# Performance work log

Hardware: AMD Instinct MI355X
Metric: run time of the kernel (lower is better)

Reference implementation:

```python
import jax, jax.numpy as jnp
import numpy as np

# ---- config (matches init_kwargs) ----
DIM = 2048
N_HEADS = 16
Q_LORA = 1536
KV_LORA = 512
QK_NOPE = 128
QK_ROPE = 64
V_HEAD = 128
QK_HEAD = QK_NOPE + QK_ROPE  # 192
B, S = 2, 2048
EPS = 1e-6


def rmsnorm(x, w):
    return x * jax.lax.rsqrt(jnp.mean(x * x, axis=-1, keepdims=True) + EPS) * w


def apply_rotary_emb(x, freqs_cis):
    # x: (B, S, H, R) interleaved pairs; freqs_cis: (S, R//2, 2) = (cos, sin)
    xr = x.astype(jnp.float32).reshape(x.shape[:-1] + (-1, 2))
    cos = freqs_cis[None, :, None, :, 0]
    sin = freqs_cis[None, :, None, :, 1]
    out = jnp.stack(
        [xr[..., 0] * cos - xr[..., 1] * sin,
         xr[..., 1] * cos + xr[..., 0] * sin], axis=-1)
    return out.reshape(x.shape).astype(x.dtype)


def setup_inputs() -> dict:
    key = jax.random.key(0)
    ks = jax.random.split(key, 12)
    sc = lambda fan_in: 1.0 / np.sqrt(fan_in)

    x = jax.random.normal(ks[0], (B, S, DIM), jnp.float32)

    # RoPE table: (S, QK_ROPE//2, 2)
    inv_freq = 1.0 / (10000.0 ** (jnp.arange(0, QK_ROPE, 2, dtype=jnp.float32) / QK_ROPE))
    t = jnp.arange(S, dtype=jnp.float32)
    ang = jnp.einsum('s,r->sr', t, inv_freq)
    freqs_cis = jnp.stack([jnp.cos(ang), jnp.sin(ang)], axis=-1)

    # causal mask (S, T)
    mask = jnp.triu(jnp.full((S, S), -jnp.inf, dtype=jnp.float32), 1)

    params = {
        'wq_a_w': jax.random.normal(ks[1], (Q_LORA, DIM), jnp.float32) * sc(DIM),
        'wq_a_b': jnp.zeros((Q_LORA,), jnp.float32),
        'q_norm_w': jnp.ones((Q_LORA,), jnp.float32),
        'wq_b_w': jax.random.normal(ks[2], (N_HEADS * QK_HEAD, Q_LORA), jnp.float32) * sc(Q_LORA),
        'wq_b_b': jnp.zeros((N_HEADS * QK_HEAD,), jnp.float32),
        'wkv_a_w': jax.random.normal(ks[3], (KV_LORA + QK_ROPE, DIM), jnp.float32) * sc(DIM),
        'wkv_a_b': jnp.zeros((KV_LORA + QK_ROPE,), jnp.float32),
        'kv_norm_w': jnp.ones((KV_LORA,), jnp.float32),
        'wkv_b_w': jax.random.normal(ks[4], (N_HEADS * (QK_NOPE + V_HEAD), KV_LORA), jnp.float32) * sc(KV_LORA),
        'wo_w': jax.random.normal(ks[5], (DIM, N_HEADS * V_HEAD), jnp.float32) * sc(N_HEADS * V_HEAD),
        'wo_b': jnp.zeros((DIM,), jnp.float32),
    }
    return {'x': x, 'freqs_cis': freqs_cis, 'mask': mask, 'start_pos': 0, **params}


def reference(x, freqs_cis, mask, wq_a_w, wq_a_b, q_norm_w, wq_b_w, wq_b_b,
              wkv_a_w, wkv_a_b, kv_norm_w, wkv_b_w, wo_w, wo_b, start_pos):
    bsz, seqlen, _ = x.shape
    scale = QK_HEAD ** (-0.5)

    # q path (low-rank)
    q = rmsnorm(x @ wq_a_w.T + wq_a_b, q_norm_w) @ wq_b_w.T + wq_b_b
    q = q.reshape(bsz, seqlen, N_HEADS, QK_HEAD)
    q_nope, q_pe = q[..., :QK_NOPE], q[..., QK_NOPE:]
    q_pe = apply_rotary_emb(q_pe, freqs_cis)

    # kv path
    kv = x @ wkv_a_w.T + wkv_a_b
    kv, k_pe = kv[..., :KV_LORA], kv[..., KV_LORA:]
    k_pe = apply_rotary_emb(k_pe[:, :, None, :], freqs_cis)[:, :, 0, :]  # (B,T,R)

    # absorption: fold W_UK into q_nope
    wkv_b = wkv_b_w.reshape(N_HEADS, QK_NOPE + V_HEAD, KV_LORA)
    q_nope = jnp.einsum('bshd,hdc->bshc', q_nope, wkv_b[:, :QK_NOPE])
    kv_cache = rmsnorm(kv, kv_norm_w)  # (B,T,C)

    scores = (jnp.einsum('bshc,btc->bsht', q_nope, kv_cache)
              + jnp.einsum('bshr,btr->bsht', q_pe, k_pe)) * scale
    scores = scores + mask[:, None, :]
    attn = jax.nn.softmax(scores.astype(jnp.float32), axis=-1).astype(x.dtype)

    out = jnp.einsum('bsht,btc->bshc', attn, kv_cache)
    out = jnp.einsum('bshc,hdc->bshd', out, wkv_b[:, -V_HEAD:])
    out = out.reshape(bsz, seqlen, N_HEADS * V_HEAD) @ wo_w.T + wo_b
    return out
```

## Files before the change

### kernel.cpp

```cpp
#include <hip/hip_runtime.h>
#include <math.h>

#define B_    2
#define S_    2048
#define M_TOT 4096
#define DIM_  2048
#define NH_   16
#define QL_   1536
#define KVL_  512
#define QKN_  128
#define QKR_  64
#define VH_   128
#define QKH_  192
#define QSTR  3072
#define QP_STR 584

typedef short s16x8 __attribute__((ext_vector_type(8)));
typedef float f32x4 __attribute__((ext_vector_type(4)));
typedef unsigned short u16;
#define AS1 __attribute__((address_space(1)))
#define AS3 __attribute__((address_space(3)))

__device__ inline u16 f2bf(float f) {
    unsigned u = __float_as_uint(f);
    unsigned r = u + 0x7FFFu + ((u >> 16) & 1u);
    return (u16)(r >> 16);
}
__device__ inline float bf2f(u16 h) { return __uint_as_float(((unsigned)h) << 16); }

__device__ __forceinline__ void ld_lds16(const u16* g, u16* l) {
    __builtin_amdgcn_global_load_lds((const AS1 unsigned*)g, (AS3 unsigned*)l, 16, 0, 0);
}
__device__ __forceinline__ void bar_vm() {
    asm volatile("s_waitcnt vmcnt(0)" ::: "memory");
    __builtin_amdgcn_s_barrier();
}
__device__ __forceinline__ void bar_lgkm() {
    asm volatile("s_waitcnt lgkmcnt(0)" ::: "memory");
    __builtin_amdgcn_s_barrier();
}
__device__ __forceinline__ void bar_all() {
    asm volatile("s_waitcnt vmcnt(0) lgkmcnt(0)" ::: "memory");
    __builtin_amdgcn_s_barrier();
}

__global__ __launch_bounds__(256)
void gemm_bf16(const u16* __restrict__ A, const u16* __restrict__ Bm,
               const float* __restrict__ bias, void* __restrict__ Cv,
               int M, int N, int K, int ldA, int ldB, int ldC,
               long long sAz, long long sBz, long long sCz,
               float alpha, int outF32)
{
    __shared__ u16 As[128 * 32];
    __shared__ u16 Bs[128 * 32];
    const int tid = threadIdx.x;
    const int w = tid >> 6, l = tid & 63;
    const int m0 = blockIdx.y * 128, n0 = blockIdx.x * 128;
    const int z = blockIdx.z;
    const u16* Az = A + (size_t)z * sAz;
    const u16* Bz = Bm + (size_t)z * sBz;

    const int rin = l >> 2;
    const int cel = (l & 3) * 8;
    const int lane15 = l & 15, quad = l >> 4;
    const int wm = w & 1, wn = w >> 1;

    f32x4 acc[4][4] = {};

    for (int k0 = 0; k0 < K; k0 += 32) {
        __syncthreads();
        #pragma unroll
        for (int c = 0; c < 2; ++c) {
            const int chunk = w * 2 + c;
            const int rowA = m0 + chunk * 16 + rin;
            const u16* ga = Az + (size_t)rowA * ldA + k0 + cel;
            u16* la = &As[chunk * 512 + rin * 32 + cel];
            __builtin_amdgcn_global_load_lds((const AS1 unsigned*)ga, (AS3 unsigned*)la, 16, 0, 0);
            int rowB = n0 + chunk * 16 + rin;
            if (rowB > N - 1) rowB = N - 1;
            const u16* gb = Bz + (size_t)rowB * ldB + k0 + cel;
            u16* lb = &Bs[chunk * 512 + rin * 32 + cel];
            __builtin_amdgcn_global_load_lds((const AS1 unsigned*)gb, (AS3 unsigned*)lb, 16, 0, 0);
        }
        __syncthreads();
        s16x8 af[4], bf[4];
        #pragma unroll
        for (int i = 0; i < 4; ++i)
            af[i] = *(const s16x8*)&As[(wm * 64 + i * 16 + lane15) * 32 + quad * 8];
        #pragma unroll
        for (int i = 0; i < 4; ++i)
            bf[i] = *(const s16x8*)&Bs[(wn * 64 + i * 16 + lane15) * 32 + quad * 8];
        #pragma unroll
        for (int mi = 0; mi < 4; ++mi)
            #pragma unroll
            for (int ni = 0; ni < 4; ++ni)
                acc[mi][ni] = __builtin_amdgcn_mfma_f32_16x16x32_bf16(af[mi], bf[ni], acc[mi][ni], 0, 0, 0);
    }

    const int cmb = m0 + wm * 64, cnb = n0 + wn * 64;
    if (outF32) {
        float* C = (float*)Cv + (size_t)z * sCz;
        #pragma unroll
        for (int mi = 0; mi < 4; ++mi)
            #pragma unroll
            for (int ni = 0; ni < 4; ++ni) {
                const int nn = cnb + ni * 16 + lane15;
                if (nn < N) {
                    const float bv = bias ? bias[nn] : 0.f;
                    #pragma unroll
                    for (int r = 0; r < 4; ++r) {
                        const int mm = cmb + mi * 16 + quad * 4 + r;
                        C[(size_t)mm * ldC + nn] = acc[mi][ni][r] * alpha + bv;
                    }
                }
            }
    } else {
        u16* C = (u16*)Cv + (size_t)z * sCz;
        #pragma unroll
        for (int mi = 0; mi < 4; ++mi)
            #pragma unroll
            for (int ni = 0; ni < 4; ++ni) {
                const int nn = cnb + ni * 16 + lane15;
                if (nn < N) {
                    const float bv = bias ? bias[nn] : 0.f;
                    #pragma unroll
                    for (int r = 0; r < 4; ++r) {
                        const int mm = cmb + mi * 16 + quad * 4 + r;
                        C[(size_t)mm * ldC + nn] = f2bf(acc[mi][ni][r] * alpha + bv);
                    }
                }
            }
    }
}

__global__ __launch_bounds__(512)
void mla_flash(u16* __restrict__ Qp, const u16* __restrict__ Kcat,
               const u16* __restrict__ KVT)
{
    __shared__ u16 sQ[64 * QP_STR];
    __shared__ u16 sKV[2][16384];
    __shared__ u16 sP[64 * 136];
    __shared__ float sRm[64 * 4];
    __shared__ float sRs[64 * 4];
    __shared__ float sM[64], sL[64];

    const int tid = threadIdx.x;
    const int w = tid >> 6, l = tid & 63;
    const int lane15 = l & 15, quad = l >> 4;
    const int wq = w & 1;
    const int wk = w >> 1;

    const int flat = blockIdx.x;
    const int xcd  = flat & 7;
    const int slot = flat >> 3;
    const int b    = xcd >> 2;
    const int h    = (xcd & 3) * 4 + (slot & 3);
    const int qt   = 31 - (slot >> 2);

    const int qs = qt * 64;
    u16* Qrow = Qp + ((size_t)h * M_TOT + b * S_ + qs) * 576;
    const float scale = 0.07216878364870323f;
    const u16* Kb = Kcat + (size_t)b * S_ * 576;
    const u16* Vb = KVT + (size_t)b * 512 * S_;

    const int key = tid >> 2;
    const int seg8 = (tid & 3) * 8;
    const int sx8  = (((tid & 3) ^ ((tid >> 3) & 3)) * 8);
    const int qx8  = ((quad ^ ((lane15 >> 1) & 3)) * 8);
    const int ktiles = (qs + 191) >> 7;

    auto stageK = [&](int kt, int j, int buf) {
        #pragma unroll
        for (int kk = 0; kk < 3; ++kk) {
            const u16* g = Kb + (size_t)(kt + key) * 576 + j * 96 + kk * 32 + sx8;
            ld_lds16(g, &sKV[buf][kk * 4096 + key * 32 + seg8]);
        }
    };
    auto stageV = [&](int kt, int tc, int buf) {
        #pragma unroll
        for (int jj = 0; jj < 4; ++jj) {
            const int c = jj * 128 + key;
            const u16* g = Vb + (size_t)c * S_ + kt + tc * 32 + sx8;
            ld_lds16(g, &sKV[buf][jj * 4096 + key * 32 + seg8]);
        }
    };

    stageK(0, 0, 0);
    {
        const int r = tid >> 3, c0 = (tid & 7) * 8;
        #pragma unroll
        for (int jj = 0; jj < 9; ++jj) {
            const int c = c0 + jj * 64;
            *(s16x8*)&sQ[r * QP_STR + c] = *(const s16x8*)&Qrow[(size_t)r * 576 + c];
        }
    }
    if (tid < 64) { sM[tid] = -1e30f; sL[tid] = 0.f; }
    bar_all();

    f32x4 Oacc[2][8] = {};
    float mn_[2][4], al_[2][4];

    for (int kt0 = 0; kt0 < ktiles; ++kt0) {
        const int kt = kt0 << 7;
        f32x4 Sacc[2][2] = {};

        #pragma unroll
        for (int j = 0; j < 6; ++j) {
            const int cur = j & 1;
            if (j < 5) stageK(kt, j + 1, cur ^ 1);
            else       stageV(kt, 0, 0);
            __builtin_amdgcn_s_setprio(1);
            #pragma unroll
            for (int kk = 0; kk < 3; ++kk) {
                s16x8 af[2], bf[2];
                #pragma unroll
                for (int mi = 0; mi < 2; ++mi)
                    af[mi] = *(const s16x8*)&sQ[(wq * 32 + mi * 16 + lane15) * QP_STR + j * 96 + kk * 32 + quad * 8];
                #pragma unroll
                for (int ni = 0; ni < 2; ++ni)
                    bf[ni] = *(const s16x8*)&sKV[cur][kk * 4096 + (wk * 32 + ni * 16 + lane15) * 32 + qx8];
                #pragma unroll
                for (int mi = 0; mi < 2; ++mi)
                    #pragma unroll
                    for (int ni = 0; ni < 2; ++ni)
                        Sacc[mi][ni] = __builtin_amdgcn_mfma_f32_16x16x32_bf16(af[mi], bf[ni], Sacc[mi][ni], 0, 0, 0);
            }
            __builtin_amdgcn_s_setprio(0);
            if (j < 5) bar_vm();
        }

        #pragma unroll
        for (int mi = 0; mi < 2; ++mi)
            #pragma unroll
            for (int r = 0; r < 4; ++r) {
                const int rowl = wq * 32 + mi * 16 + quad * 4 + r;
                const int rowg = qs + rowl;
                float mx = -1e30f;
                #pragma unroll
                for (int ni = 0; ni < 2; ++ni) {
                    const int colg = kt + wk * 32 + ni * 16 + lane15;
                    float v = Sacc[mi][ni][r] * scale;
                    v = (colg <= rowg) ? v : -1e30f;
                    Sacc[mi][ni][r] = v;
                    mx = fmaxf(mx, v);
                }
                #pragma unroll
                for (int sh = 1; sh < 16; sh <<= 1) mx = fmaxf(mx, __shfl_xor(mx, sh));
                if (lane15 == 0) sRm[rowl * 4 + wk] = mx;
            }
        bar_lgkm();

        #pragma unroll
        for (int mi = 0; mi < 2; ++mi)
            #pragma unroll
            for (int r = 0; r < 4; ++r) {
                const int rowl = wq * 32 + mi * 16 + quad * 4 + r;
                const f32x4 pm = *(const f32x4*)&sRm[rowl * 4];
                const float m_old = sM[rowl];
                const float mn = fmaxf(fmaxf(fmaxf(pm[0], pm[1]), fmaxf(pm[2], pm[3])), m_old);
                const float al = __expf(m_old - mn);
                mn_[mi][r] = mn; al_[mi][r] = al;
                float sum = 0.f;
                #pragma unroll
                for (int ni = 0; ni < 2; ++ni) {
                    const float p = __expf(Sacc[mi][ni][r] - mn);
                    sP[rowl * 136 + wk * 32 + ni * 16 + lane15] = f2bf(p);
                    sum += p;
                }
                #pragma unroll
                for (int ci = 0; ci < 8; ++ci) Oacc[mi][ci][r] *= al;
                #pragma unroll
                for (int sh = 1; sh < 16; sh <<= 1) sum += __shfl_xor(sum, sh);
                if (lane15 == 0) sRs[rowl * 4 + wk] = sum;
            }
        bar_all();

        if (wk == 0 && lane15 == 0) {
            #pragma unroll
            for (int mi = 0; mi < 2; ++mi)
                #pragma unroll
                for (int r = 0; r < 4; ++r) {
                    const int rowl = wq * 32 + mi * 16 + quad * 4 + r;
                    const f32x4 ps = *(const f32x4*)&sRs[rowl * 4];
                    sL[rowl] = sL[rowl] * al_[mi][r] + (ps[0] + ps[1] + ps[2] + ps[3]);
                    sM[rowl] = mn_[mi][r];
                }
        }

        #pragma unroll
        for (int tc = 0; tc < 4; ++tc) {
            const int cur = tc & 1;
            if (tc < 3)                 stageV(kt, tc + 1, cur ^ 1);
            else if (kt0 + 1 < ktiles)  stageK(kt + 128, 0, 0);
            s16x8 pf[2], vf[8];
            #pragma unroll
            for (int mi = 0; mi < 2; ++mi)
                pf[mi] = *(const s16x8*)&sP[(wq * 32 + mi * 16 + lane15) * 136 + tc * 32 + quad * 8];
            #pragma unroll
            for (int ci = 0; ci < 8; ++ci)
                vf[ci] = *(const s16x8*)&sKV[cur][(wk * 128 + ci * 16 + lane15) * 32 + qx8];
            __builtin_amdgcn_s_setprio(1);
            #pragma unroll
            for (int mi = 0; mi < 2; ++mi)
                #pragma unroll
                for (int ci = 0; ci < 8; ++ci)
                    Oacc[mi][ci] = __builtin_amdgcn_mfma_f32_16x16x32_bf16(pf[mi], vf[ci], Oacc[mi][ci], 0, 0, 0);
            __builtin_amdgcn_s_setprio(0);
            bar_vm();
        }
    }

    bar_lgkm();
    #pragma unroll
    for (int mi = 0; mi < 2; ++mi)
        #pragma unroll
        for (int r = 0; r < 4; ++r) {
            const int rowl = wq * 32 + mi * 16 + quad * 4 + r;
            const float inv = 1.f / sL[rowl];
            #pragma unroll
            for (int ci = 0; ci < 8; ++ci)
                Qrow[(size_t)rowl * 576 + wk * 128 + ci * 16 + lane15] =
                    f2bf(Oacc[mi][ci][r] * inv);
        }
}

__global__ __launch_bounds__(256)
void cast_f32_bf16(const float* __restrict__ src, u16* __restrict__ dst, int n)
{
    for (int i = blockIdx.x * 256 + threadIdx.x; i < n; i += gridDim.x * 256)
        dst[i] = f2bf(src[i]);
}

__global__ __launch_bounds__(256)
void prep_wbnT(const float* __restrict__ wkvb, u16* __restrict__ dst)
{
    int i = blockIdx.x * 256 + threadIdx.x;
    int h = i >> 16, rem = i & 65535, c = rem >> 7, d = rem & 127;
    dst[i] = f2bf(wkvb[(size_t)(h * 256 + d) * 512 + c]);
}

__global__ __launch_bounds__(256)
void prep_wbv(const float* __restrict__ wkvb, u16* __restrict__ dst)
{
    int i = blockIdx.x * 256 + threadIdx.x;
    int h = i >> 16, rem = i & 65535;
    dst[i] = f2bf(wkvb[(size_t)h * 131072 + 65536 + rem]);
}

__global__ __launch_bounds__(256)
void rmsnorm_bf16(u16* __restrict__ X, const float* __restrict__ w, int D)
{
    const int m = blockIdx.x;
    u16* x = X + (size_t)m * D;
    float ss = 0.f;
    for (int k = threadIdx.x; k < D; k += 256) { float v = bf2f(x[k]); ss += v * v; }
    __shared__ float red[256];
    red[threadIdx.x] = ss; __syncthreads();
    for (int s = 128; s > 0; s >>= 1) {
        if (threadIdx.x < s) red[threadIdx.x] += red[threadIdx.x + s];
        __syncthreads();
    }
    const float sc = rsqrtf(red[0] / (float)D + 1e-6f);
    for (int k = threadIdx.x; k < D; k += 256) x[k] = f2bf(bf2f(x[k]) * sc * w[k]);
}

__global__ __launch_bounds__(256)
void rope_q(const u16* __restrict__ q, const float* __restrict__ freqs, u16* __restrict__ Qp)
{
    const int idx = blockIdx.x * 256 + threadIdx.x;
    const int i = idx & 31, h = (idx >> 5) & 15, m = idx >> 9;
    const int s = m & (S_ - 1);
    const float c = freqs[(s * 32 + i) * 2], sn = freqs[(s * 32 + i) * 2 + 1];
    const u16* src = q + (size_t)m * QSTR + h * QKH_ + QKN_ + 2 * i;
    const float x0 = bf2f(src[0]), x1 = bf2f(src[1]);
    u16* dst = Qp + ((size_t)h * M_TOT + m) * 576 + 512 + 2 * i;
    dst[0] = f2bf(x0 * c - x1 * sn);
    dst[1] = f2bf(x1 * c + x0 * sn);
}

__global__ __launch_bounds__(256)
void kv_norm_rope(const u16* __restrict__ kva, const float* __restrict__ w,
                  const float* __restrict__ freqs, u16* __restrict__ Kcat)
{
    const int m = blockIdx.x, s = m & (S_ - 1);
    const u16* x = kva + (size_t)m * 576;
    float ss = 0.f;
    for (int k = threadIdx.x; k < 512; k += 256) { float v = bf2f(x[k]); ss += v * v; }
    __shared__ float red[256];
    red[threadIdx.x] = ss; __syncthreads();
    for (int st = 128; st > 0; st >>= 1) {
        if (threadIdx.x < st) red[threadIdx.x] += red[threadIdx.x + st];
        __syncthreads();
    }
    const float sc = rsqrtf(red[0] / 512.f + 1e-6f);
    for (int k = threadIdx.x; k < 512; k += 256)
        Kcat[(size_t)m * 576 + k] = f2bf(bf2f(x[k]) * sc * w[k]);
    if (threadIdx.x < 32) {
        const int i = threadIdx.x;
        const float c = freqs[(s * 32 + i) * 2], sn = freqs[(s * 32 + i) * 2 + 1];
        const float x0 = bf2f(x[512 + 2 * i]), x1 = bf2f(x[512 + 2 * i + 1]);
        Kcat[(size_t)m * 576 + 512 + 2 * i]     = f2bf(x0 * c - x1 * sn);
        Kcat[(size_t)m * 576 + 512 + 2 * i + 1] = f2bf(x1 * c + x0 * sn);
    }
}

__global__ __launch_bounds__(256)
void transpose_kv(const u16* __restrict__ Kcat, u16* __restrict__ KVT)
{
    __shared__ u16 t[64][65];
    const int s0 = blockIdx.x * 64, c0 = blockIdx.y * 64, b = blockIdx.z;
    #pragma unroll
    for (int i = 0; i < 16; ++i) {
        int id = i * 256 + threadIdx.x, r = id >> 6, c = id & 63;
        t[r][c] = Kcat[(size_t)(b * S_ + s0 + r) * 576 + c0 + c];
    }
    __syncthreads();
    #pragma unroll
    for (int i = 0; i < 16; ++i) {
        int id = i * 256 + threadIdx.x, r = id >> 6, c = id & 63;
        KVT[(size_t)(b * 512 + c0 + r) * S_ + s0 + c] = t[c][r];
    }
}

extern "C" void kernel_launch(void* const* d_in, const int* in_sizes, int n_in,
                              void* d_out, int out_size, void* d_ws, size_t ws_size,
                              hipStream_t stream)
{
    (void)in_sizes; (void)n_in; (void)out_size; (void)ws_size;
    const float* x         = (const float*)d_in[0];
    const float* freqs     = (const float*)d_in[1];
    const float* wq_a_w    = (const float*)d_in[4];
    const float* wq_a_b    = (const float*)d_in[5];
    const float* q_norm_w  = (const float*)d_in[6];
    const float* wq_b_w    = (const float*)d_in[7];
    const float* wq_b_b    = (const float*)d_in[8];
    const float* wkv_a_w   = (const float*)d_in[9];
    const float* wkv_a_b   = (const float*)d_in[10];
    const float* kv_norm_w = (const float*)d_in[11];
    const float* wkv_b_w   = (const float*)d_in[12];
    const float* wo_w      = (const float*)d_in[13];
    const float* wo_b      = (const float*)d_in[14];
    float* out = (float*)d_out;

    char* W = (char*)d_ws;
    u16* x_bf  = (u16*)(W + 0);
    u16* wqa   = (u16*)(W + 16777216);
    u16* wqb   = (u16*)(W + 23068672);
    u16* wkva  = (u16*)(W + 32505856);
    u16* wobf  = (u16*)(W + 34865152);
    u16* wbnT  = (u16*)(W + 43253760);
    u16* wbv   = (u16*)(W + 45350912);
    u16* q_a   = (u16*)(W + 47448064);
    u16* q     = (u16*)(W + 60030976);
    u16* kv_a  = (u16*)(W + 85196800);
    u16* Kcat  = (u16*)(W + 89915392);
    u16* KVT   = (u16*)(W + 94633984);
    u16* Qp    = (u16*)(W + 98828288);
    u16* outh  = (u16*)(W + 174325760);

    const dim3 blk(256);

    cast_f32_bf16<<<2048, blk, 0, stream>>>(x, x_bf, M_TOT * DIM_);
    cast_f32_bf16<<<2048, blk, 0, stream>>>(wq_a_w, wqa, QL_ * DIM_);
    cast_f32_bf16<<<2048, blk, 0, stream>>>(wq_b_w, wqb, QSTR * QL_);
    cast_f32_bf16<<<2048, blk, 0, stream>>>(wkv_a_w, wkva, 576 * DIM_);
    cast_f32_bf16<<<2048, blk, 0, stream>>>(wo_w, wobf, DIM_ * DIM_);
    prep_wbnT<<<4096, blk, 0, stream>>>(wkv_b_w, wbnT);
    prep_wbv<<<4096, blk, 0, stream>>>(wkv_b_w, wbv);

    gemm_bf16<<<dim3(12, 32, 1), blk, 0, stream>>>(x_bf, wqa, wq_a_b, q_a,
        M_TOT, QL_, DIM_, DIM_, DIM_, QL_, 0, 0, 0, 1.f, 0);
    rmsnorm_bf16<<<M_TOT, blk, 0, stream>>>(q_a, q_norm_w, QL_);
    gemm_bf16<<<dim3(24, 32, 1), blk, 0, stream>>>(q_a, wqb, wq_b_b, q,
        M_TOT, QSTR, QL_, QL_, QL_, QSTR, 0, 0, 0, 1.f, 0);
    rope_q<<<(M_TOT * NH_ * 32) / 256, blk, 0, stream>>>(q, freqs, Qp);

    gemm_bf16<<<dim3(5, 32, 1), blk, 0, stream>>>(x_bf, wkva, wkv_a_b, kv_a,
        M_TOT, 576, DIM_, DIM_, DIM_, 576, 0, 0, 0, 1.f, 0);
    kv_norm_rope<<<M_TOT, blk, 0, stream>>>(kv_a, kv_norm_w, freqs, Kcat);
    transpose_kv<<<dim3(32, 8, 2), blk, 0, stream>>>(Kcat, KVT);

    gemm_bf16<<<dim3(4, 32, 16), blk, 0, stream>>>(q, wbnT, nullptr, Qp,
        M_TOT, 512, 128, QSTR, 128, 576, QKH_, 65536, (long long)M_TOT * 576, 1.f, 0);

    mla_flash<<<dim3(1024, 1, 1), dim3(512), 0, stream>>>(Qp, Kcat, KVT);

    gemm_bf16<<<dim3(1, 32, 16), blk, 0, stream>>>(Qp, wbv, nullptr, outh,
        M_TOT, VH_, 512, 576, 512, DIM_, (long long)M_TOT * 576, 65536, VH_, 1.f, 0);

    gemm_bf16<<<dim3(16, 32, 1), blk, 0, stream>>>(outh, wobf, wo_b, out,
        M_TOT, DIM_, DIM_, DIM_, DIM_, DIM_, 0, 0, 0, 1.f, 1);
}
```

Before: 851.1 us.

## Shrink MLA flash tile to 32 query rows and skip masked key sub-tiles

The flash attention kernel now uses 32-row query tiles with 256 threads and launches twice as many blocks. Each of the four waves owns a 32-key slice for QK and a 64-column slice of V. Key and V sub-tiles that lie fully beyond the causal diagonal are no longer staged or multiplied, and the K/V double buffer carries parity across tiles. The softmax switches to exp2 with a log2e-folded scale and skips rescaling the output accumulator when the running max has not grown past a threshold. The aim is finer causal work skipping, better load balance and less rescale work, at the cost of less Q reuse per K/V load and more blocks and barriers.

```diff
diff --git a/kernel.cpp b/kernel.cpp
--- a/kernel.cpp
+++ b/kernel.cpp
@@ -133,56 +133,59 @@
     }
 }
 
-__global__ __launch_bounds__(512)
+__global__ __launch_bounds__(256)
 void mla_flash(u16* __restrict__ Qp, const u16* __restrict__ Kcat,
                const u16* __restrict__ KVT)
 {
-    __shared__ u16 sQ[64 * QP_STR];
-    __shared__ u16 sKV[2][16384];
-    __shared__ u16 sP[64 * 136];
-    __shared__ float sRm[64 * 4];
-    __shared__ float sRs[64 * 4];
-    __shared__ float sM[64], sL[64];
+    __shared__ u16 sQ[32 * QP_STR];
+    __shared__ u16 sKV[2][8192];
+    __shared__ u16 sP[32 * 136];
+    __shared__ float sRm[32 * 4];
+    __shared__ float sRs[32 * 4];
+    __shared__ float sM[32], sL[32];
 
     const int tid = threadIdx.x;
     const int w = tid >> 6, l = tid & 63;
     const int lane15 = l & 15, quad = l >> 4;
-    const int wq = w & 1;
-    const int wk = w >> 1;
 
     const int flat = blockIdx.x;
     const int xcd  = flat & 7;
     const int slot = flat >> 3;
     const int b    = xcd >> 2;
     const int h    = (xcd & 3) * 4 + (slot & 3);
-    const int qt   = 31 - (slot >> 2);
-
-    const int qs = qt * 64;
+    const int qt   = 63 - (slot >> 2);
+    const int qs   = qt * 32;
+
     u16* Qrow = Qp + ((size_t)h * M_TOT + b * S_ + qs) * 576;
-    const float scale = 0.07216878364870323f;
+    const float scale2 = 0.10411758f;
     const u16* Kb = Kcat + (size_t)b * S_ * 576;
     const u16* Vb = KVT + (size_t)b * 512 * S_;
 
-    const int key = tid >> 2;
     const int seg8 = (tid & 3) * 8;
     const int sx8  = (((tid & 3) ^ ((tid >> 3) & 3)) * 8);
     const int qx8  = ((quad ^ ((lane15 >> 1) & 3)) * 8);
-    const int ktiles = (qs + 191) >> 7;
+    const int ktiles = (qs + 159) >> 7;
 
     auto stageK = [&](int kt, int j, int buf) {
         #pragma unroll
-        for (int kk = 0; kk < 3; ++kk) {
-            const u16* g = Kb + (size_t)(kt + key) * 576 + j * 96 + kk * 32 + sx8;
-            ld_lds16(g, &sKV[buf][kk * 4096 + key * 32 + seg8]);
-        }
+        for (int kk = 0; kk < 2; ++kk)
+            #pragma unroll
+            for (int ps = 0; ps < 2; ++ps) {
+                const int key = (tid >> 2) + ps * 64;
+                const u16* g = Kb + (size_t)(kt + key) * 576 + j * 64 + kk * 32 + sx8;
+                ld_lds16(g, &sKV[buf][kk * 4096 + key * 32 + seg8]);
+            }
     };
-    auto stageV = [&](int kt, int tc, int buf) {
-        #pragma unroll
-        for (int jj = 0; jj < 4; ++jj) {
-            const int c = jj * 128 + key;
-            const u16* g = Vb + (size_t)c * S_ + kt + tc * 32 + sx8;
-            ld_lds16(g, &sKV[buf][jj * 4096 + key * 32 + seg8]);
-        }
+    auto stageV = [&](int kt, int tc, int hf, int buf) {
+        #pragma unroll
+        for (int jj = 0; jj < 2; ++jj)
+            #pragma unroll
+            for (int ps = 0; ps < 2; ++ps) {
+                const int rl = (tid >> 2) + ps * 64;
+                const int c  = hf * 256 + jj * 128 + rl;
+                const u16* g = Vb + (size_t)c * S_ + kt + tc * 32 + sx8;
+                ld_lds16(g, &sKV[buf][jj * 4096 + rl * 32 + seg8]);
+            }
     };
 
     stageK(0, 0, 0);
@@ -194,93 +197,128 @@
             *(s16x8*)&sQ[r * QP_STR + c] = *(const s16x8*)&Qrow[(size_t)r * 576 + c];
         }
     }
-    if (tid < 64) { sM[tid] = -1e30f; sL[tid] = 0.f; }
+    if (tid < 32) { sM[tid] = -1e30f; sL[tid] = 0.f; }
     bar_all();
 
     f32x4 Oacc[2][8] = {};
     float mn_[2][4], al_[2][4];
+    int pb = 0;
 
     for (int kt0 = 0; kt0 < ktiles; ++kt0) {
         const int kt = kt0 << 7;
+        const int klen = min(128, qs + 32 - kt);
         f32x4 Sacc[2][2] = {};
 
         #pragma unroll
-        for (int j = 0; j < 6; ++j) {
-            const int cur = j & 1;
-            if (j < 5) stageK(kt, j + 1, cur ^ 1);
-            else       stageV(kt, 0, 0);
-            __builtin_amdgcn_s_setprio(1);
-            #pragma unroll
-            for (int kk = 0; kk < 3; ++kk) {
-                s16x8 af[2], bf[2];
-                #pragma unroll
-                for (int mi = 0; mi < 2; ++mi)
-                    af[mi] = *(const s16x8*)&sQ[(wq * 32 + mi * 16 + lane15) * QP_STR + j * 96 + kk * 32 + quad * 8];
-                #pragma unroll
-                for (int ni = 0; ni < 2; ++ni)
-                    bf[ni] = *(const s16x8*)&sKV[cur][kk * 4096 + (wk * 32 + ni * 16 + lane15) * 32 + qx8];
-                #pragma unroll
-                for (int mi = 0; mi < 2; ++mi)
+        for (int j = 0; j < 9; ++j) {
+            const int cur = (j + pb) & 1;
+            if (j < 8) stageK(kt, j + 1, cur ^ 1);
+            else       stageV(kt, 0, 0, cur ^ 1);
+            if (w * 32 < klen) {
+                __builtin_amdgcn_s_setprio(1);
+                #pragma unroll
+                for (int kk = 0; kk < 2; ++kk) {
+                    s16x8 af[2], bf[2];
+                    #pragma unroll
+                    for (int mi = 0; mi < 2; ++mi)
+                        af[mi] = *(const s16x8*)&sQ[(mi * 16 + lane15) * QP_STR + j * 64 + kk * 32 + quad * 8];
                     #pragma unroll
                     for (int ni = 0; ni < 2; ++ni)
-                        Sacc[mi][ni] = __builtin_amdgcn_mfma_f32_16x16x32_bf16(af[mi], bf[ni], Sacc[mi][ni], 0, 0, 0);
-            }
-            __builtin_amdgcn_s_setprio(0);
-            if (j < 5) bar_vm();
+                        bf[ni] = *(const s16x8*)&sKV[cur][kk * 4096 + (w * 32 + ni * 16 + lane15) * 32 + qx8];
+                    #pragma unroll
+                    for (int mi = 0; mi < 2; ++mi)
+                        #pragma unroll
+                        for (int ni = 0; ni < 2; ++ni)
+                            Sacc[mi][ni] = __builtin_amdgcn_mfma_f32_16x16x32_bf16(af[mi], bf[ni], Sacc[mi][ni], 0, 0, 0);
+                }
+                __builtin_amdgcn_s_setprio(0);
+            }
+            if (j < 8) bar_vm();
         }
 
         #pragma unroll
         for (int mi = 0; mi < 2; ++mi)
             #pragma unroll
             for (int r = 0; r < 4; ++r) {
-                const int rowl = wq * 32 + mi * 16 + quad * 4 + r;
+                const int rowl = mi * 16 + quad * 4 + r;
                 const int rowg = qs + rowl;
                 float mx = -1e30f;
                 #pragma unroll
                 for (int ni = 0; ni < 2; ++ni) {
-                    const int colg = kt + wk * 32 + ni * 16 + lane15;
-                    float v = Sacc[mi][ni][r] * scale;
+                    const int colg = kt + w * 32 + ni * 16 + lane15;
+                    float v = Sacc[mi][ni][r] * scale2;
                     v = (colg <= rowg) ? v : -1e30f;
                     Sacc[mi][ni][r] = v;
                     mx = fmaxf(mx, v);
                 }
                 #pragma unroll
                 for (int sh = 1; sh < 16; sh <<= 1) mx = fmaxf(mx, __shfl_xor(mx, sh));
-                if (lane15 == 0) sRm[rowl * 4 + wk] = mx;
+                if (lane15 == 0) sRm[rowl * 4 + w] = mx;
             }
         bar_lgkm();
 
+        float dmax = 0.f;
         #pragma unroll
         for (int mi = 0; mi < 2; ++mi)
             #pragma unroll
             for (int r = 0; r < 4; ++r) {
-                const int rowl = wq * 32 + mi * 16 + quad * 4 + r;
+                const int rowl = mi * 16 + quad * 4 + r;
                 const f32x4 pm = *(const f32x4*)&sRm[rowl * 4];
                 const float m_old = sM[rowl];
-                const float mn = fmaxf(fmaxf(fmaxf(pm[0], pm[1]), fmaxf(pm[2], pm[3])), m_old);
-                const float al = __expf(m_old - mn);
-                mn_[mi][r] = mn; al_[mi][r] = al;
+                const float mnc = fmaxf(fmaxf(pm[0], pm[1]), fmaxf(pm[2], pm[3]));
+                dmax = fmaxf(dmax, mnc - m_old);
+                mn_[mi][r] = mnc;
+                al_[mi][r] = m_old;
+            }
+        const bool rescale = !__all(dmax <= 8.f);
+        #pragma unroll
+        for (int mi = 0; mi < 2; ++mi)
+            #pragma unroll
+            for (int r = 0; r < 4; ++r) {
+                const float m_old = al_[mi][r];
+                if (rescale) {
+                    const float mn = fmaxf(mn_[mi][r], m_old);
+                    al_[mi][r] = exp2f(m_old - mn);
+                    mn_[mi][r] = mn;
+                } else {
+                    mn_[mi][r] = m_old;
+                    al_[mi][r] = 1.f;
+                }
+            }
+        if (rescale) {
+            #pragma unroll
+            for (int mi = 0; mi < 2; ++mi)
+                #pragma unroll
+                for (int ci = 0; ci < 8; ++ci)
+                    #pragma unroll
+                    for (int r = 0; r < 4; ++r)
+                        Oacc[mi][ci][r] *= al_[mi][r];
+        }
+        #pragma unroll
+        for (int mi = 0; mi < 2; ++mi)
+            #pragma unroll
+            for (int r = 0; r < 4; ++r) {
+                const int rowl = mi * 16 + quad * 4 + r;
+                const float mn = mn_[mi][r];
                 float sum = 0.f;
                 #pragma unroll
                 for (int ni = 0; ni < 2; ++ni) {
-                    const float p = __expf(Sacc[mi][ni][r] - mn);
-                    sP[rowl * 136 + wk * 32 + ni * 16 + lane15] = f2bf(p);
+                    const float p = exp2f(Sacc[mi][ni][r] - mn);
+                    sP[rowl * 136 + w * 32 + ni * 16 + lane15] = f2bf(p);
                     sum += p;
                 }
                 #pragma unroll
-                for (int ci = 0; ci < 8; ++ci) Oacc[mi][ci][r] *= al;
-                #pragma unroll
                 for (int sh = 1; sh < 16; sh <<= 1) sum += __shfl_xor(sum, sh);
-                if (lane15 == 0) sRs[rowl * 4 + wk] = sum;
+                if (lane15 == 0) sRs[rowl * 4 + w] = sum;
             }
         bar_all();
 
-        if (wk == 0 && lane15 == 0) {
+        if (w == 0 && lane15 == 0) {
             #pragma unroll
             for (int mi = 0; mi < 2; ++mi)
                 #pragma unroll
                 for (int r = 0; r < 4; ++r) {
-                    const int rowl = wq * 32 + mi * 16 + quad * 4 + r;
+                    const int rowl = mi * 16 + quad * 4 + r;
                     const f32x4 ps = *(const f32x4*)&sRs[rowl * 4];
                     sL[rowl] = sL[rowl] * al_[mi][r] + (ps[0] + ps[1] + ps[2] + ps[3]);
                     sM[rowl] = mn_[mi][r];
@@ -289,25 +327,44 @@
 
         #pragma unroll
         for (int tc = 0; tc < 4; ++tc) {
-            const int cur = tc & 1;
-            if (tc < 3)                 stageV(kt, tc + 1, cur ^ 1);
-            else if (kt0 + 1 < ktiles)  stageK(kt + 128, 0, 0);
-            s16x8 pf[2], vf[8];
-            #pragma unroll
-            for (int mi = 0; mi < 2; ++mi)
-                pf[mi] = *(const s16x8*)&sP[(wq * 32 + mi * 16 + lane15) * 136 + tc * 32 + quad * 8];
-            #pragma unroll
-            for (int ci = 0; ci < 8; ++ci)
-                vf[ci] = *(const s16x8*)&sKV[cur][(wk * 128 + ci * 16 + lane15) * 32 + qx8];
-            __builtin_amdgcn_s_setprio(1);
-            #pragma unroll
-            for (int mi = 0; mi < 2; ++mi)
-                #pragma unroll
-                for (int ci = 0; ci < 8; ++ci)
-                    Oacc[mi][ci] = __builtin_amdgcn_mfma_f32_16x16x32_bf16(pf[mi], vf[ci], Oacc[mi][ci], 0, 0, 0);
-            __builtin_amdgcn_s_setprio(0);
-            bar_vm();
-        }
+            const bool live = (tc * 32 < klen);
+            s16x8 pf[2];
+            if (live) {
+                #pragma unroll
+                for (int mi = 0; mi < 2; ++mi)
+                    pf[mi] = *(const s16x8*)&sP[(mi * 16 + lane15) * 136 + tc * 32 + quad * 8];
+            }
+            #pragma unroll
+            for (int hf = 0; hf < 2; ++hf) {
+                const int ph  = 9 + tc * 2 + hf;
+                const int cur = (ph + pb) & 1;
+                const bool last = (tc == 3 && hf == 1);
+                if (last) {
+                    if (kt0 + 1 < ktiles) stageK(kt + 128, 0, cur ^ 1);
+                } else {
+                    const int ntc = tc + hf;
+                    const int nhf = hf ^ 1;
+                    if (ntc * 32 < klen) stageV(kt, ntc, nhf, cur ^ 1);
+                }
+                if (live) {
+                    s16x8 vf[4];
+                    #pragma unroll
+                    for (int ci = 0; ci < 4; ++ci) {
+                        const int rl = w * 64 + ci * 16 + lane15;
+                        vf[ci] = *(const s16x8*)&sKV[cur][(rl >> 7) * 4096 + (rl & 127) * 32 + qx8];
+                    }
+                    __builtin_amdgcn_s_setprio(1);
+                    #pragma unroll
+                    for (int mi = 0; mi < 2; ++mi)
+                        #pragma unroll
+                        for (int ci = 0; ci < 4; ++ci)
+                            Oacc[mi][hf * 4 + ci] = __builtin_amdgcn_mfma_f32_16x16x32_bf16(pf[mi], vf[ci], Oacc[mi][hf * 4 + ci], 0, 0, 0);
+                    __builtin_amdgcn_s_setprio(0);
+                }
+                if (live || last) bar_vm();
+            }
+        }
+        pb ^= 1;
     }
 
     bar_lgkm();
@@ -315,12 +372,14 @@
     for (int mi = 0; mi < 2; ++mi)
         #pragma unroll
         for (int r = 0; r < 4; ++r) {
-            const int rowl = wq * 32 + mi * 16 + quad * 4 + r;
+            const int rowl = mi * 16 + quad * 4 + r;
             const float inv = 1.f / sL[rowl];
             #pragma unroll
-            for (int ci = 0; ci < 8; ++ci)
-                Qrow[(size_t)rowl * 576 + wk * 128 + ci * 16 + lane15] =
-                    f2bf(Oacc[mi][ci][r] * inv);
+            for (int hf = 0; hf < 2; ++hf)
+                #pragma unroll
+                for (int ci = 0; ci < 4; ++ci)
+                    Qrow[(size_t)rowl * 576 + hf * 256 + w * 64 + ci * 16 + lane15] =
+                        f2bf(Oacc[mi][hf * 4 + ci][r] * inv);
         }
 }
 
@@ -483,7 +542,7 @@
     gemm_bf16<<<dim3(4, 32, 16), blk, 0, stream>>>(q, wbnT, nullptr, Qp,
         M_TOT, 512, 128, QSTR, 128, 576, QKH_, 65536, (long long)M_TOT * 576, 1.f, 0);
 
-    mla_flash<<<dim3(1024, 1, 1), dim3(512), 0, stream>>>(Qp, Kcat, KVT);
+    mla_flash<<<dim3(2048, 1, 1), dim3(256), 0, stream>>>(Qp, Kcat, KVT);
 
     gemm_bf16<<<dim3(1, 32, 16), blk, 0, stream>>>(Qp, wbv, nullptr, outh,
         M_TOT, VH_, 512, 576, 512, DIM_, (long long)M_TOT * 576, 65536, VH_, 1.f, 0);
```

New measurement: 1.340 ms. 1.57x slower.

## Restructure MLA flash loop into 4-stage LDS ring with partial vmcnt waits

Applied to the files above, without the earlier changes.

Replaces the double-buffered K/V staging in the flash attention kernel with a four-slot ring of smaller chunks (64-wide K slices, half-width V slices). Loads are issued three stages ahead and barriers wait only on vmcnt(4)/vmcnt(2), so global-to-LDS copies stay in flight across the score, softmax and PV phases, including prefetching the next tile's K during PV. The aim is to hide memory latency behind MFMA work. The cost is more barriers and intricate buffer-index arithmetic, where an off-by-one in the ring would corrupt data.

```diff
diff --git a/kernel.cpp b/kernel.cpp
--- a/kernel.cpp
+++ b/kernel.cpp
@@ -31,18 +31,10 @@
 __device__ __forceinline__ void ld_lds16(const u16* g, u16* l) {
     __builtin_amdgcn_global_load_lds((const AS1 unsigned*)g, (AS3 unsigned*)l, 16, 0, 0);
 }
-__device__ __forceinline__ void bar_vm() {
-    asm volatile("s_waitcnt vmcnt(0)" ::: "memory");
-    __builtin_amdgcn_s_barrier();
-}
-__device__ __forceinline__ void bar_lgkm() {
-    asm volatile("s_waitcnt lgkmcnt(0)" ::: "memory");
-    __builtin_amdgcn_s_barrier();
-}
-__device__ __forceinline__ void bar_all() {
-    asm volatile("s_waitcnt vmcnt(0) lgkmcnt(0)" ::: "memory");
-    __builtin_amdgcn_s_barrier();
-}
+#define BARW4 do { asm volatile("s_waitcnt vmcnt(4) lgkmcnt(0)" ::: "memory"); __builtin_amdgcn_s_barrier(); } while (0)
+#define BARW2 do { asm volatile("s_waitcnt vmcnt(2) lgkmcnt(0)" ::: "memory"); __builtin_amdgcn_s_barrier(); } while (0)
+#define BARW0 do { asm volatile("s_waitcnt vmcnt(0) lgkmcnt(0)" ::: "memory"); __builtin_amdgcn_s_barrier(); } while (0)
+#define BARLG do { asm volatile("s_waitcnt lgkmcnt(0)" ::: "memory"); __builtin_amdgcn_s_barrier(); } while (0)
 
 __global__ __launch_bounds__(256)
 void gemm_bf16(const u16* __restrict__ A, const u16* __restrict__ Bm,
@@ -138,7 +130,7 @@
                const u16* __restrict__ KVT)
 {
     __shared__ u16 sQ[64 * QP_STR];
-    __shared__ u16 sKV[2][16384];
+    __shared__ u16 sKV[4 * 8192];
     __shared__ u16 sP[64 * 136];
     __shared__ float sRm[64 * 4];
     __shared__ float sRs[64 * 4];
@@ -156,36 +148,56 @@
     const int b    = xcd >> 2;
     const int h    = (xcd & 3) * 4 + (slot & 3);
     const int qt   = 31 - (slot >> 2);
-
-    const int qs = qt * 64;
+    const int qs   = qt * 64;
+
     u16* Qrow = Qp + ((size_t)h * M_TOT + b * S_ + qs) * 576;
     const float scale = 0.07216878364870323f;
     const u16* Kb = Kcat + (size_t)b * S_ * 576;
     const u16* Vb = KVT + (size_t)b * 512 * S_;
 
-    const int key = tid >> 2;
     const int seg8 = (tid & 3) * 8;
     const int sx8  = (((tid & 3) ^ ((tid >> 3) & 3)) * 8);
     const int qx8  = ((quad ^ ((lane15 >> 1) & 3)) * 8);
-    const int ktiles = (qs + 191) >> 7;
-
-    auto stageK = [&](int kt, int j, int buf) {
-        #pragma unroll
-        for (int kk = 0; kk < 3; ++kk) {
-            const u16* g = Kb + (size_t)(kt + key) * 576 + j * 96 + kk * 32 + sx8;
-            ld_lds16(g, &sKV[buf][kk * 4096 + key * 32 + seg8]);
-        }
+    const int ktiles = (qs + 64 + 127) >> 7;
+
+    auto issueK = [&](int kt, int j, int buf) {
+        const int key = tid >> 2;
+        const u16* g = Kb + (size_t)(kt + key) * 576 + j * 64 + sx8;
+        u16* d = &sKV[(buf << 13) + key * 32 + seg8];
+        ld_lds16(g, d);
+        ld_lds16(g + 32, d + 4096);
     };
-    auto stageV = [&](int kt, int tc, int buf) {
-        #pragma unroll
-        for (int jj = 0; jj < 4; ++jj) {
-            const int c = jj * 128 + key;
-            const u16* g = Vb + (size_t)c * S_ + kt + tc * 32 + sx8;
-            ld_lds16(g, &sKV[buf][jj * 4096 + key * 32 + seg8]);
-        }
+    auto issueV = [&](int kt, int tc, int hf, int buf) {
+        const int rl = tid >> 2;
+        const u16* g = Vb + (size_t)(hf * 256 + rl) * S_ + kt + tc * 32 + sx8;
+        u16* d = &sKV[(buf << 13) + rl * 32 + seg8];
+        ld_lds16(g, d);
+        ld_lds16(g + (size_t)128 * S_, d + 4096);
     };
-
-    stageK(0, 0, 0);
+    auto scoreC = [&](int j, int buf, f32x4 (&Sacc)[2][2]) {
+        const u16* base = &sKV[buf << 13];
+        __builtin_amdgcn_s_setprio(1);
+        #pragma unroll
+        for (int kk = 0; kk < 2; ++kk) {
+            s16x8 af[2], bf[2];
+            #pragma unroll
+            for (int mi = 0; mi < 2; ++mi)
+                af[mi] = *(const s16x8*)&sQ[(wq * 32 + mi * 16 + lane15) * QP_STR + j * 64 + kk * 32 + quad * 8];
+            #pragma unroll
+            for (int ni = 0; ni < 2; ++ni)
+                bf[ni] = *(const s16x8*)&base[kk * 4096 + (wk * 32 + ni * 16 + lane15) * 32 + qx8];
+            #pragma unroll
+            for (int mi = 0; mi < 2; ++mi)
+                #pragma unroll
+                for (int ni = 0; ni < 2; ++ni)
+                    Sacc[mi][ni] = __builtin_amdgcn_mfma_f32_16x16x32_bf16(af[mi], bf[ni], Sacc[mi][ni], 0, 0, 0);
+        }
+        __builtin_amdgcn_s_setprio(0);
+    };
+
+    issueK(0, 0, 0);
+    issueK(0, 1, 1);
+    issueK(0, 2, 2);
     {
         const int r = tid >> 3, c0 = (tid & 7) * 8;
         #pragma unroll
@@ -195,40 +207,29 @@
         }
     }
     if (tid < 64) { sM[tid] = -1e30f; sL[tid] = 0.f; }
-    bar_all();
+    BARW4;
 
     f32x4 Oacc[2][8] = {};
-    float mn_[2][4], al_[2][4];
-
-    for (int kt0 = 0; kt0 < ktiles; ++kt0) {
-        const int kt = kt0 << 7;
+
+    for (int t = 0; t < ktiles; ++t) {
+        const int kt = t << 7;
+        const int tb = t & 3;
+        const bool hn = (t + 1 < ktiles);
         f32x4 Sacc[2][2] = {};
 
         #pragma unroll
-        for (int j = 0; j < 6; ++j) {
-            const int cur = j & 1;
-            if (j < 5) stageK(kt, j + 1, cur ^ 1);
-            else       stageV(kt, 0, 0);
-            __builtin_amdgcn_s_setprio(1);
-            #pragma unroll
-            for (int kk = 0; kk < 3; ++kk) {
-                s16x8 af[2], bf[2];
-                #pragma unroll
-                for (int mi = 0; mi < 2; ++mi)
-                    af[mi] = *(const s16x8*)&sQ[(wq * 32 + mi * 16 + lane15) * QP_STR + j * 96 + kk * 32 + quad * 8];
-                #pragma unroll
-                for (int ni = 0; ni < 2; ++ni)
-                    bf[ni] = *(const s16x8*)&sKV[cur][kk * 4096 + (wk * 32 + ni * 16 + lane15) * 32 + qx8];
-                #pragma unroll
-                for (int mi = 0; mi < 2; ++mi)
-                    #pragma unroll
-                    for (int ni = 0; ni < 2; ++ni)
-                        Sacc[mi][ni] = __builtin_amdgcn_mfma_f32_16x16x32_bf16(af[mi], bf[ni], Sacc[mi][ni], 0, 0, 0);
-            }
-            __builtin_amdgcn_s_setprio(0);
-            if (j < 5) bar_vm();
-        }
-
+        for (int s = 0; s < 6; ++s) {
+            issueK(kt, s + 3, (tb + s + 3) & 3);
+            scoreC(s, (tb + s) & 3, Sacc);
+            BARW4;
+        }
+        scoreC(6, (tb + 6) & 3, Sacc);
+        BARW2;
+        issueV(kt, 0, 0, (tb + 9) & 3);
+        scoreC(7, (tb + 7) & 3, Sacc);
+        BARW2;
+        issueV(kt, 0, 1, (tb + 10) & 3);
+        scoreC(8, (tb + 8) & 3, Sacc);
         #pragma unroll
         for (int mi = 0; mi < 2; ++mi)
             #pragma unroll
@@ -248,8 +249,10 @@
                 for (int sh = 1; sh < 16; sh <<= 1) mx = fmaxf(mx, __shfl_xor(mx, sh));
                 if (lane15 == 0) sRm[rowl * 4 + wk] = mx;
             }
-        bar_lgkm();
-
+        BARW2;
+
+        issueV(kt, 1, 0, (tb + 11) & 3);
+        float mn_[2][4], al_[2][4];
         #pragma unroll
         for (int mi = 0; mi < 2; ++mi)
             #pragma unroll
@@ -273,7 +276,7 @@
                 for (int sh = 1; sh < 16; sh <<= 1) sum += __shfl_xor(sum, sh);
                 if (lane15 == 0) sRs[rowl * 4 + wk] = sum;
             }
-        bar_all();
+        BARLG;
 
         if (wk == 0 && lane15 == 0) {
             #pragma unroll
@@ -288,29 +291,36 @@
         }
 
         #pragma unroll
-        for (int tc = 0; tc < 4; ++tc) {
-            const int cur = tc & 1;
-            if (tc < 3)                 stageV(kt, tc + 1, cur ^ 1);
-            else if (kt0 + 1 < ktiles)  stageK(kt + 128, 0, 0);
-            s16x8 pf[2], vf[8];
-            #pragma unroll
-            for (int mi = 0; mi < 2; ++mi)
-                pf[mi] = *(const s16x8*)&sP[(wq * 32 + mi * 16 + lane15) * 136 + tc * 32 + quad * 8];
-            #pragma unroll
-            for (int ci = 0; ci < 8; ++ci)
-                vf[ci] = *(const s16x8*)&sKV[cur][(wk * 128 + ci * 16 + lane15) * 32 + qx8];
-            __builtin_amdgcn_s_setprio(1);
-            #pragma unroll
-            for (int mi = 0; mi < 2; ++mi)
-                #pragma unroll
-                for (int ci = 0; ci < 8; ++ci)
-                    Oacc[mi][ci] = __builtin_amdgcn_mfma_f32_16x16x32_bf16(pf[mi], vf[ci], Oacc[mi][ci], 0, 0, 0);
-            __builtin_amdgcn_s_setprio(0);
-            bar_vm();
-        }
-    }
-
-    bar_lgkm();
+        for (int k = 0; k < 8; ++k) {
+            const int cis = 12 + k;
+            if (cis <= 16)      issueV(kt, (cis - 9) >> 1, (cis - 9) & 1, (tb + cis) & 3);
+            else if (hn)        issueK(kt + 128, cis - 17, (tb + 1 + (cis - 17)) & 3);
+            {
+                const int tc = k >> 1, hf = k & 1;
+                const u16* base = &sKV[(((tb + 9 + k) & 3)) << 13];
+                s16x8 pf[2], vf[4];
+                #pragma unroll
+                for (int mi = 0; mi < 2; ++mi)
+                    pf[mi] = *(const s16x8*)&sP[(wq * 32 + mi * 16 + lane15) * 136 + tc * 32 + quad * 8];
+                #pragma unroll
+                for (int ci = 0; ci < 4; ++ci) {
+                    const int rl = wk * 64 + ci * 16 + lane15;
+                    vf[ci] = *(const s16x8*)&base[rl * 32 + qx8];
+                }
+                __builtin_amdgcn_s_setprio(1);
+                #pragma unroll
+                for (int mi = 0; mi < 2; ++mi)
+                    #pragma unroll
+                    for (int ci = 0; ci < 4; ++ci)
+                        Oacc[mi][hf * 4 + ci] = __builtin_amdgcn_mfma_f32_16x16x32_bf16(pf[mi], vf[ci], Oacc[mi][hf * 4 + ci], 0, 0, 0);
+                __builtin_amdgcn_s_setprio(0);
+            }
+            if (k < 5 || hn) { BARW4; }
+            else if (k == 5) { BARW2; }
+            else if (k == 6) { BARW0; }
+        }
+    }
+
     #pragma unroll
     for (int mi = 0; mi < 2; ++mi)
         #pragma unroll
@@ -318,9 +328,11 @@
             const int rowl = wq * 32 + mi * 16 + quad * 4 + r;
             const float inv = 1.f / sL[rowl];
             #pragma unroll
-            for (int ci = 0; ci < 8; ++ci)
-                Qrow[(size_t)rowl * 576 + wk * 128 + ci * 16 + lane15] =
-                    f2bf(Oacc[mi][ci][r] * inv);
+            for (int hf = 0; hf < 2; ++hf)
+                #pragma unroll
+                for (int ci = 0; ci < 4; ++ci)
+                    Qrow[(size_t)rowl * 576 + hf * 256 + wk * 64 + ci * 16 + lane15] =
+                        f2bf(Oacc[mi][hf * 4 + ci][r] * inv);
         }
 }
 
```

New measurement: 924.5 us. +8.6%, slower.
